# Kernel tuning notes

Hardware: AMD Instinct MI355X
Metric: run time of the kernel (lower is better)

Reference implementation:

```python
import jax, jax.numpy as jnp
import numpy as np

EPS = 1e-7
MIN_NORM = 1e-15
MAX_NORM = 1e6


def _arcosh(x):
    return jnp.log(x + jnp.sqrt(jnp.clip(x * x - 1.0, EPS, None)))


def _mink_dot(x, y):
    # Minkowski inner product <x,y>_L, keepdim
    return jnp.sum(x * y, axis=-1, keepdims=True) - 2.0 * x[..., 0:1] * y[..., 0:1]


def _mink_norm(u):
    return jnp.sqrt(jnp.clip(_mink_dot(u, u), EPS, None))


def _proj(x, c):
    K = 1.0 / c
    y = x[..., 1:]
    first = jnp.sqrt(jnp.clip(K + jnp.sum(y * y, axis=-1, keepdims=True), EPS, None))
    return jnp.concatenate([first, y], axis=-1)


def _proj_tan(u, x, c):
    ux = jnp.sum(x[..., 1:] * u[..., 1:], axis=-1, keepdims=True)
    first = ux / jnp.clip(x[..., 0:1], EPS, None)
    return jnp.concatenate([first, u[..., 1:]], axis=-1)


def _logmap0(x, c):
    K = 1.0 / c
    sqrtK = jnp.sqrt(K)
    y = x[..., 1:]
    y_norm = jnp.clip(jnp.linalg.norm(y, axis=-1, keepdims=True), MIN_NORM, None)
    theta = jnp.clip(x[..., 0:1] / sqrtK, 1.0 + EPS, None)
    return jnp.concatenate([jnp.zeros_like(theta), sqrtK * _arcosh(theta) * y / y_norm], axis=-1)


def _expmap0(u, c):
    K = 1.0 / c
    sqrtK = jnp.sqrt(K)
    x = u[..., 1:]
    x_norm = jnp.clip(jnp.linalg.norm(x, axis=-1, keepdims=True), MIN_NORM, None)
    theta = x_norm / sqrtK
    return jnp.concatenate([sqrtK * jnp.cosh(theta), sqrtK * jnp.sinh(theta) * x / x_norm], axis=-1)


def _expmap(u, x, c):
    K = 1.0 / c
    sqrtK = jnp.sqrt(K)
    theta = jnp.clip(jnp.clip(_mink_norm(u), None, MAX_NORM) / sqrtK, MIN_NORM, None)
    return _proj(jnp.cosh(theta) * x + jnp.sinh(theta) * u / theta, c)


def _ptransp0(x, u, c):
    K = 1.0 / c
    sqrtK = jnp.sqrt(K)
    x0 = x[..., 0:1]
    y = x[..., 1:]
    y_norm = jnp.clip(jnp.linalg.norm(y, axis=-1, keepdims=True), MIN_NORM, None)
    y_hat = y / y_norm
    v = jnp.concatenate([-y_norm, (sqrtK - x0) * y_hat], axis=-1)
    alpha = jnp.sum(y_hat * u[..., 1:], axis=-1, keepdims=True) / sqrtK
    return _proj_tan(u - alpha * v, x, c)


def _mobius_add(x, y, c):
    u = _logmap0(y, c)
    v = _ptransp0(x, u, c)
    return _expmap(v, x, c)


def _mobius_matvec(m, x, c):
    # rev=False: left-multiply tangent vectors by m
    return _expmap0(m @ _logmap0(x, c), c)


def _sqdist(x, y, c):
    K = 1.0 / c
    theta = jnp.clip(-_mink_dot(x, y) / K, 1.0 + EPS, None)
    return jnp.clip(K * _arcosh(theta) ** 2, None, 50.0)


def _h2k(x):
    return x[..., 1:] / x[..., 0:1]


def _k2h(x):
    sq = jnp.clip(jnp.sum(x * x, axis=-1, keepdims=True), None, 0.999)
    return jnp.concatenate([jnp.ones_like(x[..., 0:1]), x], axis=-1) / jnp.sqrt(1.0 - sq)


def _lorenz_factor(x):
    # default c=1.0 (the learnable c is NOT passed here in the original)
    sq = jnp.clip(jnp.sum(x * x, axis=-1, keepdims=True), None, 0.9)
    return 1.0 / jnp.sqrt(1.0 - sq)


def _one_transform(W, h, b, c):
    n, t, d = h.shape
    # faithful raw row-major reshape (NOT a transpose), matching torch.reshape
    Wh = _mobius_matvec(W, h.reshape(t, n * d), c).reshape(n * t, d)
    return _proj(_mobius_add(Wh, b, c), c)


def setup_inputs() -> dict:
    key = jax.random.key(0)
    n, t, d = 8192, 16, 64
    ks = jax.random.split(key, 3)
    # valid hyperboloid points (c=1): x0 = sqrt(1 + |y|^2)
    y = 0.5 * jax.random.normal(ks[0], (n, t, d - 1), jnp.float32)
    x0 = jnp.sqrt(1.0 + jnp.sum(y * y, axis=-1, keepdims=True))
    big_h = jnp.concatenate([x0, y], axis=-1)
    # all causal time pairs (m, nn<=m) so every segment of the scatter is non-empty
    pairs = np.array([(m, nn) for m in range(t) for nn in range(m + 1)], dtype=np.int64)
    time_index = jnp.asarray(pairs.T)  # (2, 136)
    E = time_index.shape[1]
    mask = jnp.zeros((1, E, 1), jnp.float32)
    lim = float(np.sqrt(6.0 / (t + t)))  # glorot
    w_q = jax.random.uniform(ks[1], (t, t), jnp.float32, -lim, lim)
    w_k = jax.random.uniform(ks[2], (t, t), jnp.float32, -lim, lim)
    b_q = jnp.ones((1, d), jnp.float32)
    b_k = jnp.ones((1, d), jnp.float32)
    a = jnp.ones((1,), jnp.float32)
    c = jnp.ones((1,), jnp.float32)
    return {"big_h": big_h, "time_index": time_index, "mask": mask,
            "w_q": w_q, "w_k": w_k, "b_q": b_q, "b_k": b_k, "a": a, "c": c}


def reference(big_h, time_index, mask, w_q, w_k, b_q, b_k, a, c):
    n, t, d = big_h.shape
    t_m = time_index[0]
    t_n = time_index[1]
    q = _one_transform(w_q, big_h, b_q, c).reshape(n, t, d)
    k = _one_transform(w_k, big_h, b_k, c).reshape(n, t, d)
    v = _h2k(big_h.reshape(n * t, d)).reshape(n, t, d - 1)  # Klein coords
    dist = -_sqdist(q[:, t_m, :], k[:, t_n, :], c)          # (n, E, 1)
    s = jnp.exp(a * dist - c + mask)
    s_sum = jnp.zeros((n, t, 1), s.dtype).at[:, t_m, :].add(s)
    beta = s / s_sum[:, t_n, :]                              # segment softmax
    lamb = _lorenz_factor(v.reshape(n * t, d - 1)).reshape(n, t, 1)[:, t_n, :]
    v_tn = v[:, t_n, :]
    z = v_tn * lamb * beta
    w = lamb * beta
    z_sum = jnp.zeros((n, t, d - 1), z.dtype).at[:, t_m, :].add(z)
    w_sum = jnp.zeros((n, t, 1), w.dtype).at[:, t_m, :].add(w)
    out = z_sum / w_sum                                       # Einstein midpoint
    return _k2h(out.reshape(n * t, d - 1)).reshape(n, t, d)
```

## Files before the change

kernel.cpp:

```cpp
#include <hip/hip_runtime.h>
#include <stdint.h>

typedef unsigned short u16;
typedef unsigned int   u32;

#define EPSF  1e-7f
#define MINN  1e-15f

#define CPR  524288
#define NE   136
#define QS   68
#define VS   68
#define CMS  17
#define NBANK 7

#define WQP 952
#define WKP 1208
#define SCQ 1464
#define SCK 1480
#define CHQ 1496
#define CHK 1512
#define UQ  1528
#define UK  1592

__device__ __forceinline__ float bf2f(u16 u){ u32 x = ((u32)u)<<16; return __uint_as_float(x); }
__device__ __forceinline__ float ldv(const void* p, size_t i, int f32m){
    return f32m ? ((const float*)p)[i] : bf2f(((const u16*)p)[i]);
}
__device__ __forceinline__ float arcosh_f(float x){
    return logf(x + sqrtf(fmaxf(x*x - 1.0f, EPSF)));
}
__device__ __forceinline__ float clampf(float v, float lim){
    return fmaxf(fminf(v, lim), -lim);
}
__device__ __forceinline__ float red16(float v){
    v += __shfl_xor(v,1); v += __shfl_xor(v,2);
    v += __shfl_xor(v,4); v += __shfl_xor(v,8);
    return v;
}
__device__ __forceinline__ int detect_f32(const void* Hv){
    const float* Hf = (const float*)Hv;
    int ok = 1;
#pragma unroll
    for(int i=0;i<16;i++){
        float v = Hf[(size_t)i*1024];
        if(!(v > 0.9f && v < 1000.f)) ok = 0;
    }
    return ok;
}

__device__ __forceinline__ void load_tile(const void* Hv, int f32m, int i0, int c0, float4* hx){
    if(f32m){
        const float* Hf = (const float*)Hv;
#pragma unroll
        for(int s=0;s<16;s++) hx[s] = *(const float4*)(Hf + ((size_t)(512*s + i0))*1024 + c0);
    } else {
        const u16* Hu = (const u16*)Hv;
#pragma unroll
        for(int s=0;s<16;s++){
            ushort4 u4 = *(const ushort4*)(Hu + ((size_t)(512*s + i0))*1024 + c0);
            hx[s] = make_float4(bf2f(u4.x), bf2f(u4.y), bf2f(u4.z), bf2f(u4.w));
        }
    }
}

template<int G>
__device__ __forceinline__ void gram_body(const float4* hx, float* acc){
    int p=0;
#pragma unroll
    for(int s=0;s<16;s++){
#pragma unroll
        for(int s2=s;s2<16;s2++){
            if(p >= 34*G && p < 34*G+34){
                acc[p-34*G] = hx[s].x*hx[s2].x + hx[s].y*hx[s2].y
                            + hx[s].z*hx[s2].z + hx[s].w*hx[s2].w;
            }
            p++;
        }
    }
}

__global__ __launch_bounds__(256) void gram3_k(const void* __restrict__ Hv, float* __restrict__ ws){
    __shared__ float gred[34];
    const int tid = threadIdx.x;
    const int g   = blockIdx.x >> 9;
    const int i0  = blockIdx.x & 511;
    const int f32m = detect_f32(Hv);
    const int c0 = tid*4;

    float4 hx[16];
    load_tile(Hv, f32m, i0, c0, hx);

    float acc[34];
    switch(g){
        case 0: gram_body<0>(hx, acc); break;
        case 1: gram_body<1>(hx, acc); break;
        case 2: gram_body<2>(hx, acc); break;
        default: gram_body<3>(hx, acc); break;
    }

    if(tid<34) gred[tid]=0.f;
    __syncthreads();
#pragma unroll
    for(int j=0;j<34;j++){
        float v=acc[j];
        v+=__shfl_xor(v,1);  v+=__shfl_xor(v,2);  v+=__shfl_xor(v,4);
        v+=__shfl_xor(v,8);  v+=__shfl_xor(v,16); v+=__shfl_xor(v,32);
        if((tid&63)==0) atomicAdd(&gred[j], v);
    }
    __syncthreads();
    if(tid<34) atomicAdd(&ws[(i0%NBANK)*NE + 34*g + tid], gred[tid]);
}

__global__ void fin4_k(const void* __restrict__ Hv, const void* __restrict__ wq, const void* __restrict__ wk,
                       const void* __restrict__ bq, const void* __restrict__ bk, const void* __restrict__ cc,
                       float* __restrict__ ws){
    __shared__ float Gy[16][17], alpha[16], h0s[16], wqp[256], wkp[256], aus[2];
    const int tid = threadIdx.x;
    const int row = tid>>4, l = tid&15;
    const int f32m = detect_f32(Hv);
    float cv = fmaxf(ldv(cc,0,f32m), 1e-20f);
    float K = 1.f/cv, sqK = sqrtf(K);
    if(tid<16) h0s[tid] = ldv(Hv, (size_t)tid*CPR, f32m);
    __syncthreads();
    if(tid<NE){
        int s=0, rem=tid;
        while(rem >= 16 - s){ rem -= 16 - s; s++; }
        int s2 = s + rem;
        float gsum = 0.f;
#pragma unroll
        for(int b=0;b<NBANK;b++) gsum += ws[b*NE+tid];
        float g = gsum - h0s[s]*h0s[s2];
        Gy[s][s2] = g; Gy[s2][s] = g;
    }
    __syncthreads();
    if(tid<16){
        float ny = fmaxf(sqrtf(fmaxf(Gy[tid][tid],0.f)), MINN);
        float th = fmaxf(h0s[tid]/sqK, 1.0f+EPSF);
        alpha[tid] = sqK*arcosh_f(th)/ny;
    }
    __syncthreads();
    {
        float aq = ldv(wq,tid,f32m)*alpha[l];
        float ak = ldv(wk,tid,f32m)*alpha[l];
        wqp[tid] = aq; wkp[tid] = ak;
        ws[WQP+tid] = aq; ws[WKP+tid] = ak;
    }
    if(tid<128){
        int lane = tid&63;
        const void* bb = (tid<64)? bq : bk;
        float v = (lane==0)? 0.f : ldv(bb,lane,f32m);
        float sn = v*v;
        sn += __shfl_xor(sn,1);  sn += __shfl_xor(sn,2);  sn += __shfl_xor(sn,4);
        sn += __shfl_xor(sn,8);  sn += __shfl_xor(sn,16); sn += __shfl_xor(sn,32);
        if(lane==0){
            float b0 = ldv(bb,0,f32m);
            float nb = fmaxf(sqrtf(sn), MINN);
            float th = fmaxf(b0/sqK, 1.0f+EPSF);
            aus[tid>>6] = sqK*arcosh_f(th)/nb;
        }
    }
    __syncthreads();
    {
        float innerQ = 0.f, innerK = 0.f;
#pragma unroll
        for(int s2=0;s2<16;s2++){
            float gy = Gy[l][s2];
            innerQ += wqp[row*16+s2]*gy;
            innerK += wkp[row*16+s2]*gy;
        }
        float tq = red16(wqp[row*16+l]*innerQ);
        float tk = red16(wkp[row*16+l]*innerK);
        if(l==0){
            float xn = fmaxf(sqrtf(fmaxf(tq,0.f)), MINN);
            float thc = fminf(xn/sqK, 80.f);
            ws[SCQ+row] = clampf(sqK*sinhf(thc)/xn, 1e18f);
            ws[CHQ+row] = clampf(sqK*coshf(thc),    1e18f);
            xn = fmaxf(sqrtf(fmaxf(tk,0.f)), MINN);
            thc = fminf(xn/sqK, 80.f);
            ws[SCK+row] = clampf(sqK*sinhf(thc)/xn, 1e18f);
            ws[CHK+row] = clampf(sqK*coshf(thc),    1e18f);
        }
    }
    if(tid<64){
        ws[UQ+tid] = (tid==0)?0.f : clampf(aus[0]*ldv(bq,tid,f32m), 1e18f);
        ws[UK+tid] = (tid==0)?0.f : clampf(aus[1]*ldv(bk,tid,f32m), 1e18f);
    }
}

__global__ __launch_bounds__(256,6) void main7_k(const void* __restrict__ Hv, const int* __restrict__ tidx,
        const void* __restrict__ mask, const void* __restrict__ aav, const void* __restrict__ ccv,
        const float* __restrict__ ws, float* __restrict__ out){
    __shared__ __attribute__((aligned(16))) float vrow[16*VS];
    __shared__ __attribute__((aligned(16))) float qv[16*QS];
    __shared__ __attribute__((aligned(16))) float kv[16*QS];
    __shared__ float wqp[256], wkp[256], scQ[16], scK[16], chQ[16], chK[16], uq[64], uk[64];
    __shared__ float ssum[16], Cm[16*CMS], lamb[16], invv[16];
    __shared__ int   tmv[NE], tnv[NE];
    __shared__ float maskv[NE];

    const int tid = threadIdx.x;
    const int r   = blockIdx.x >> 9;
    const int i0  = blockIdx.x & 511;
    const int row = tid>>4, l = tid&15;
    const int f32m = detect_f32(Hv);
    const float av = ldv(aav,0,f32m);
    const float cv = fmaxf(ldv(ccv,0,f32m), 1e-20f);
    const float K = 1.f/cv, sqK = sqrtf(K);
    const int i64m = (tidx[1] != 1);
    const int c0 = tid*4;

    const float* Hf = (const float*)Hv;
    const u16*   Hu = (const u16*)Hv;

    wqp[tid] = ws[WQP+tid]; wkp[tid] = ws[WKP+tid];
    if(tid<16){ scQ[tid]=ws[SCQ+tid]; scK[tid]=ws[SCK+tid]; chQ[tid]=ws[CHQ+tid]; chK[tid]=ws[CHK+tid]; }
    if(tid<64){ uq[tid]=ws[UQ+tid]; uk[tid]=ws[UK+tid]; }
    if(tid<NE){
        if(i64m){ tmv[tid]=tidx[2*tid]&15; tnv[tid]=tidx[2*NE+2*tid]&15; }
        else    { tmv[tid]=tidx[tid]&15;   tnv[tid]=tidx[NE+tid]&15; }
        maskv[tid]=ldv(mask,tid,f32m);
    }
    __syncthreads();

    float aq0=0,aq1=0,aq2=0,aq3=0, ak0=0,ak1=0,ak2=0,ak3=0;
    float4 vr;
    const int rQ = r<<4;
    if(f32m){
#define STEPF(J) { const int s_=(r+J)&15; \
        float4 b = *(const float4*)(Hf + ((size_t)(512*s_ + i0))*1024 + c0); \
        if(J==0) vr = b; \
        float wq_=wqp[rQ+s_], wk_=wkp[rQ+s_]; \
        aq0 += wq_*b.x; aq1 += wq_*b.y; aq2 += wq_*b.z; aq3 += wq_*b.w; \
        ak0 += wk_*b.x; ak1 += wk_*b.y; ak2 += wk_*b.z; ak3 += wk_*b.w; }
        STEPF(0)  STEPF(1)  STEPF(2)  STEPF(3)
        STEPF(4)  STEPF(5)  STEPF(6)  STEPF(7)
        STEPF(8)  STEPF(9)  STEPF(10) STEPF(11)
        STEPF(12) STEPF(13) STEPF(14) STEPF(15)
#undef STEPF
    } else {
#define STEPB(J) { const int s_=(r+J)&15; \
        ushort4 u4_ = *(const ushort4*)(Hu + ((size_t)(512*s_ + i0))*1024 + c0); \
        float4 b = make_float4(bf2f(u4_.x), bf2f(u4_.y), bf2f(u4_.z), bf2f(u4_.w)); \
        if(J==0) vr = b; \
        float wq_=wqp[rQ+s_], wk_=wkp[rQ+s_]; \
        aq0 += wq_*b.x; aq1 += wq_*b.y; aq2 += wq_*b.z; aq3 += wq_*b.w; \
        ak0 += wk_*b.x; ak1 += wk_*b.y; ak2 += wk_*b.z; ak3 += wk_*b.w; }
        STEPB(0)  STEPB(1)  STEPB(2)  STEPB(3)
        STEPB(4)  STEPB(5)  STEPB(6)  STEPB(7)
        STEPB(8)  STEPB(9)  STEPB(10) STEPB(11)
        STEPB(12) STEPB(13) STEPB(14) STEPB(15)
#undef STEPB
    }

    {
        float sq_ = scQ[r], sk_ = scK[r];
        float q0 = clampf(sq_*aq0,1e18f), q1=clampf(sq_*aq1,1e18f),
              q2 = clampf(sq_*aq2,1e18f), q3=clampf(sq_*aq3,1e18f);
        float k0 = clampf(sk_*ak0,1e18f), k1=clampf(sk_*ak1,1e18f),
              k2 = clampf(sk_*ak2,1e18f), k3=clampf(sk_*ak3,1e18f);
        if(i0==0 && tid==0){ q0 = chQ[r]; k0 = chK[r]; }
        *(float4*)(qv + row*QS + l*4) = make_float4(q0,q1,q2,q3);
        *(float4*)(kv + row*QS + l*4) = make_float4(k0,k1,k2,k3);
    }

    {
        *(float4*)(vrow + row*VS + l*4) = vr;
        float x0v = vrow[row*VS];
        float inv0 = 1.f/((fabsf(x0v)>1e-20f)? x0v : 1e-20f);
        float sv = 0.f;
#pragma unroll
        for(int m=0;m<4;m++){
            int kp = l + 16*m;
            if(kp < 63){ float vi = vrow[row*VS + 1 + kp]*inv0; sv += vi*vi; }
        }
        sv = red16(sv);
        if(l==0){ lamb[row] = 1.f/sqrtf(1.f - fminf(sv, 0.9f)); invv[row] = inv0; }
        if(tid<16) ssum[tid]=0.f;
        Cm[tid]=0.f;
        if(tid<16) Cm[256+tid]=0.f;
    }

    {
        float xq[4], xk[4];
        float syq=0,suq=0,syk=0,suk=0;
#pragma unroll
        for(int m=0;m<4;m++){
            int k = l+16*m;
            xq[m]=qv[row*QS+k]; xk[m]=kv[row*QS+k];
            if(k>0){ syq+=xq[m]*xq[m]; suq+=xq[m]*uq[k];
                     syk+=xk[m]*xk[m]; suk+=xk[m]*uk[k]; }
        }
        syq=red16(syq); suq=red16(suq); syk=red16(syk); suk=red16(suk);
        float x0q=qv[row*QS], x0k=kv[row*QS];
        float xnq=fmaxf(sqrtf(fmaxf(syq,0.f)),MINN);
        float xnk=fmaxf(sqrtf(fmaxf(syk,0.f)),MINN);
        float alq=clampf(suq/(xnq*sqK),1e12f);
        float alk=clampf(suk/(xnk*sqK),1e12f);
        float cfq=clampf(alq*(sqK-x0q)/xnq,1e12f);
        float cfk=clampf(alk*(sqK-x0k)/xnk,1e12f);
        float wq4[4], wk4[4];
        float uxq=0,swq=0,uxk=0,swk=0;
#pragma unroll
        for(int m=0;m<4;m++){
            int k=l+16*m;
            if(k>0){
                wq4[m]=clampf(uq[k]-cfq*xq[m],1e15f); uxq+=xq[m]*wq4[m]; swq+=wq4[m]*wq4[m];
                wk4[m]=clampf(uk[k]-cfk*xk[m],1e15f); uxk+=xk[m]*wk4[m]; swk+=wk4[m]*wk4[m];
            } else { wq4[m]=0.f; wk4[m]=0.f; }
        }
        uxq=red16(uxq); swq=red16(swq); uxk=red16(uxk); swk=red16(swk);
        float V0q=uxq/fmaxf(x0q,EPSF);
        float V0k=uxk/fmaxf(x0k,EPSF);
        float mnq=sqrtf(fmaxf(swq-V0q*V0q,EPSF));
        float mnk=sqrtf(fmaxf(swk-V0k*V0k,EPSF));
        float thq=fminf(fmaxf(fminf(mnq,1e6f)/sqK,MINN),20.f);
        float thk=fminf(fmaxf(fminf(mnk,1e6f)/sqK,MINN),20.f);
        float chq=coshf(thq), stq=sinhf(thq)/thq;
        float chk=coshf(thk), stk=sinhf(thk)/thk;
        float zq4[4], zk4[4];
        float szq=0,szk=0;
#pragma unroll
        for(int m=0;m<4;m++){
            int k=l+16*m;
            if(k>0){
                zq4[m]=clampf(chq*xq[m]+stq*wq4[m],1e15f); szq+=zq4[m]*zq4[m];
                zk4[m]=clampf(chk*xk[m]+stk*wk4[m],1e15f); szk+=zk4[m]*zk4[m];
            } else { zq4[m]=0.f; zk4[m]=0.f; }
        }
        szq=red16(szq); szk=red16(szk);
        float fq = sqrtf(fmaxf(K+szq,EPSF));
        float fk = sqrtf(fmaxf(K+szk,EPSF));
#pragma unroll
        for(int m=0;m<4;m++){
            int k=l+16*m;
            qv[row*QS+k] = (k==0)? fq : zq4[m];
            kv[row*QS+k] = (k==0)? fk : zk4[m];
        }
    }
    __syncthreads();

    if(tid<NE){
        int m = tmv[tid], nn = tnv[tid];
        const float4* qp = (const float4*)(qv + m*QS);
        const float4* kp = (const float4*)(kv + nn*QS);
        float dot = 0.f;
#pragma unroll
        for(int t4=0;t4<16;t4++){
            float4 q4 = qp[t4], k4 = kp[t4];
            dot += q4.x*k4.x + q4.y*k4.y + q4.z*k4.z + q4.w*k4.w;
        }
        float mdot = dot - 2.f*qv[m*QS]*kv[nn*QS];
        float th = fmaxf(-mdot/K, 1.0f+EPSF);
        float ac = arcosh_f(th);
        float sqd = fminf(K*ac*ac, 50.f);
        float sval = expf(fminf(-av*sqd - cv + maskv[tid], 80.f));
        Cm[m*CMS+nn] = sval;
        atomicAdd(&ssum[m], sval);
    }
    __syncthreads();

    if(tid<NE){
        int m = tmv[tid], nn = tnv[tid];
        Cm[m*CMS+nn] = lamb[nn]*Cm[m*CMS+nn]/fmaxf(ssum[nn],1e-37f);
    }
    __syncthreads();

    {
        float cs[16]; float wsm = 0.f;
#pragma unroll
        for(int s=0;s<16;s++){
            float cmv = Cm[row*CMS+s];
            wsm += cmv;
            cs[s] = cmv*invv[s];
        }
        wsm = fmaxf(wsm, 1e-37f);
        float g4[4]; float sg=0.f;
#pragma unroll
        for(int m=0;m<4;m++){
            int kp = l+16*m;
            float num = 0.f;
#pragma unroll
            for(int s=0;s<16;s++) num += cs[s]*vrow[s*VS + 1 + kp];
            float gvv = (kp<63)? num/wsm : 0.f;
            g4[m]=gvv; sg += gvv*gvv;
        }
        sg = red16(sg);
        float inv = 1.f/sqrtf(1.f - fminf(sg, 0.999f));
        size_t base = ((size_t)(512*r + i0)*16 + row)*64;
        if(l==0) out[base] = inv;
#pragma unroll
        for(int m=0;m<4;m++){
            int kp=l+16*m;
            if(kp<63) out[base+1+kp] = g4[m]*inv;
        }
    }
}

extern "C" void kernel_launch(void* const* d_in, const int* in_sizes, int n_in,
                              void* d_out, int out_size, void* d_ws, size_t ws_size,
                              hipStream_t stream){
    const void* H    = d_in[0];
    const int* tidx  = (const int*)d_in[1];
    const void* mask = d_in[2];
    const void* wq   = d_in[3];
    const void* wk   = d_in[4];
    const void* bq   = d_in[5];
    const void* bk   = d_in[6];
    const void* aa   = d_in[7];
    const void* cc   = d_in[8];
    float* out = (float*)d_out;
    float* ws  = (float*)d_ws;

    hipMemsetAsync(ws, 0, NBANK*NE*sizeof(float), stream);
    gram3_k<<<2048,256,0,stream>>>(H, ws);
    fin4_k <<<1,   256,0,stream>>>(H, wq, wk, bq, bk, cc, ws);
    main7_k<<<8192,256,0,stream>>>(H, tidx, mask, aa, cc, ws, out);
}
```

Measured before the change: 194.6 us.

## Compute all Gram groups per block and reduce through shared memory

Replaces the Gram kernel that launched four blocks per tile (one per group of 34 products) with one block per tile that computes all four groups from a single load of the tile. The per-product wave shuffle reductions and LDS atomics are replaced by a transposed shared-memory reduction over 136 threads followed by a small shuffle. This removes the 4x redundant loads of H and the long chains of shuffles, at the cost of 35 KB of LDS per block, extra syncs, and only 512 blocks, which limits parallelism.

```diff
diff --git a/kernel.cpp b/kernel.cpp
--- a/kernel.cpp
+++ b/kernel.cpp
@@ -80,36 +80,37 @@
     }
 }
 
-__global__ __launch_bounds__(256) void gram3_k(const void* __restrict__ Hv, float* __restrict__ ws){
-    __shared__ float gred[34];
+__global__ __launch_bounds__(256) void gram4_k(const void* __restrict__ Hv, float* __restrict__ ws){
+    __shared__ float red[256*35];
     const int tid = threadIdx.x;
-    const int g   = blockIdx.x >> 9;
-    const int i0  = blockIdx.x & 511;
+    const int i0  = blockIdx.x;
     const int f32m = detect_f32(Hv);
     const int c0 = tid*4;
 
     float4 hx[16];
     load_tile(Hv, f32m, i0, c0, hx);
 
-    float acc[34];
-    switch(g){
-        case 0: gram_body<0>(hx, acc); break;
-        case 1: gram_body<1>(hx, acc); break;
-        case 2: gram_body<2>(hx, acc); break;
-        default: gram_body<3>(hx, acc); break;
-    }
-
-    if(tid<34) gred[tid]=0.f;
-    __syncthreads();
-#pragma unroll
-    for(int j=0;j<34;j++){
-        float v=acc[j];
-        v+=__shfl_xor(v,1);  v+=__shfl_xor(v,2);  v+=__shfl_xor(v,4);
-        v+=__shfl_xor(v,8);  v+=__shfl_xor(v,16); v+=__shfl_xor(v,32);
-        if((tid&63)==0) atomicAdd(&gred[j], v);
-    }
-    __syncthreads();
-    if(tid<34) atomicAdd(&ws[(i0%NBANK)*NE + 34*g + tid], gred[tid]);
+#define GRAM_GROUP(G) { \
+        float acc[34]; \
+        gram_body<G>(hx, acc); \
+        _Pragma("unroll") \
+        for(int j=0;j<34;j++) red[tid*35+j] = acc[j]; \
+        __syncthreads(); \
+        if(tid < 136){ \
+            int j = tid>>2, q = tid&3; \
+            float s = 0.f; \
+            _Pragma("unroll 16") \
+            for(int t=q*64; t<q*64+64; t++) s += red[t*35 + j]; \
+            s += __shfl_xor(s,1); s += __shfl_xor(s,2); \
+            if(q==0) atomicAdd(&ws[(i0%NBANK)*NE + 34*G + j], s); \
+        } \
+        __syncthreads(); }
+
+    GRAM_GROUP(0)
+    GRAM_GROUP(1)
+    GRAM_GROUP(2)
+    GRAM_GROUP(3)
+#undef GRAM_GROUP
 }
 
 __global__ void fin4_k(const void* __restrict__ Hv, const void* __restrict__ wq, const void* __restrict__ wk,
@@ -413,7 +414,7 @@
     float* ws  = (float*)d_ws;
 
     hipMemsetAsync(ws, 0, NBANK*NE*sizeof(float), stream);
-    gram3_k<<<2048,256,0,stream>>>(H, ws);
+    gram4_k<<<512, 256,0,stream>>>(H, ws);
     fin4_k <<<1,   256,0,stream>>>(H, wq, wk, bq, bk, cc, ws);
     main7_k<<<8192,256,0,stream>>>(H, tidx, mask, aa, cc, ws, out);
 }
```

Result: faster. 179.8 us (-7.6%).
